# Optimization experiments

Measured on AMD Instinct MI355X. Metric: run time of the kernel, lower is better.

## Reference

```python
import jax, jax.numpy as jnp
import numpy as np
from jax import lax

N_HEADS = 8

def _rope(x, d, base=10000.0):
    # x: [b, h, t, c]; rotary on first d dims (neox rotate-half within d), rest passes through
    t = x.shape[2]
    theta = 1.0 / (base ** (jnp.arange(0, d, 2, dtype=jnp.float32) / d))  # [d//2]
    ang = jnp.arange(t, dtype=jnp.float32)[:, None] * theta[None, :]      # [t, d//2]
    ang = jnp.concatenate([ang, ang], axis=-1)                            # [t, d]
    cos, sin = jnp.cos(ang), jnp.sin(ang)
    xr, xp = x[..., :d], x[..., d:]
    neg = jnp.concatenate([-xr[..., d // 2:], xr[..., :d // 2]], axis=-1)
    return jnp.concatenate([xr * cos + neg * sin, xp], axis=-1)

def _conv1x1(x, W, b):
    # x [b,c,t], W [o,c,1]
    return jnp.einsum('oc,bct->bot', W[..., 0], x) + b[None, :, None]

def _conv1d(x, W, b):
    pad = W.shape[-1] // 2
    y = lax.conv_general_dilated(x, W, (1,), [(pad, pad)], dimension_numbers=('NCH', 'OIH', 'NCH'))
    return y + b[None, :, None]

def _layer_norm_c(x, gamma, beta, eps=1e-4):
    # channel-dim LayerNorm on [b,c,t]
    mean = jnp.mean(x, axis=1, keepdims=True)
    var = jnp.mean((x - mean) ** 2, axis=1, keepdims=True)
    return (x - mean) * lax.rsqrt(var + eps) * gamma[None, :, None] + beta[None, :, None]

def _forward(x, x_mask, Wq, bq, Wk, bk, Wv, bv, Wo, bo, g1, be1, W1, c1, W2, c2, g2, be2):
    B, C, T = x.shape
    H = N_HEADS
    kc = C // H
    d_rope = kc // 2
    scale = np.float32(1.0 / np.sqrt(kc))
    attn_mask = (x_mask[:, :, None, :] * x_mask[:, :, :, None]) > 0  # [B,1,T,T]

    def split(u):
        return u.reshape(B, H, kc, T).transpose(0, 1, 3, 2)  # b (h c) t -> b h t c

    for i in range(Wq.shape[0]):
        x = x * x_mask
        q = _rope(split(_conv1x1(x, Wq[i], bq[i])), d_rope)
        k = _rope(split(_conv1x1(x, Wk[i], bk[i])), d_rope)
        v = split(_conv1x1(x, Wv[i], bv[i]))
        scores = jnp.einsum('bhtc,bhsc->bhts', q, k) * scale
        scores = jnp.where(attn_mask, scores, jnp.float32(-10000.0))
        p = jax.nn.softmax(scores, axis=-1)
        o = jnp.einsum('bhts,bhsc->bhtc', p, v)
        o = o.transpose(0, 1, 3, 2).reshape(B, C, T)  # b h t c -> b (h c) t
        x = _layer_norm_c(x + _conv1x1(o, Wo[i], bo[i]), g1[i], be1[i])
        h = jax.nn.relu(_conv1d(x * x_mask, W1[i], c1[i]))
        y = _conv1d(h * x_mask, W2[i], c2[i]) * x_mask
        x = _layer_norm_c(x + y, g2[i], be2[i])
    return x * x_mask

def setup_inputs():
    key = jax.random.key(0)
    B, C, T, F, K, L = 4, 512, 1024, 2048, 3, 6
    ks = jax.random.split(key, 8)
    s = np.float32(1.0 / np.sqrt(C))
    return {
        'x': jax.random.normal(ks[0], (B, C, T), dtype=jnp.float32),
        'x_mask': jnp.ones((B, 1, T), dtype=jnp.float32),
        'Wq': jax.random.normal(ks[1], (L, C, C, 1), jnp.float32) * s,
        'bq': jnp.zeros((L, C), jnp.float32),
        'Wk': jax.random.normal(ks[2], (L, C, C, 1), jnp.float32) * s,
        'bk': jnp.zeros((L, C), jnp.float32),
        'Wv': jax.random.normal(ks[3], (L, C, C, 1), jnp.float32) * s,
        'bv': jnp.zeros((L, C), jnp.float32),
        'Wo': jax.random.normal(ks[4], (L, C, C, 1), jnp.float32) * s,
        'bo': jnp.zeros((L, C), jnp.float32),
        'g1': jnp.ones((L, C), jnp.float32),
        'be1': jnp.zeros((L, C), jnp.float32),
        'W1': jax.random.normal(ks[5], (L, F, C, K), jnp.float32) * np.float32(1.0 / np.sqrt(C * K)),
        'c1': jnp.zeros((L, F), jnp.float32),
        'W2': jax.random.normal(ks[6], (L, C, F, K), jnp.float32) * np.float32(1.0 / np.sqrt(F * K)),
        'c2': jnp.zeros((L, C), jnp.float32),
        'g2': jnp.ones((L, C), jnp.float32),
        'be2': jnp.zeros((L, C), jnp.float32),
    }

def reference(x, x_mask, Wq, bq, Wk, bk, Wv, bv, Wo, bo, g1, be1, W1, c1, W2, c2, g2, be2):
    return _forward(x, x_mask, Wq, bq, Wk, bk, Wv, bv, Wo, bo, g1, be1, W1, c1, W2, c2, g2, be2)
```

## Files before the change

### kernel.cpp

```cpp
#include <hip/hip_runtime.h>

typedef __bf16 bf16;
typedef __bf16 bf16x2 __attribute__((ext_vector_type(2)));
typedef __bf16 bf16x8 __attribute__((ext_vector_type(8)));
typedef __bf16 bf16x4v __attribute__((ext_vector_type(4)));
typedef float f32x4 __attribute__((ext_vector_type(4)));

constexpr int B = 4, C = 512, T = 1024, H = 8, F = 2048, L = 6;
constexpr int TP = T + 18;
constexpr float SCALE = 0.125f, EPS = 1e-4f;

__device__ __forceinline__ void stage_rows(const char* g, long strideB, char* lds,
                                           int nChunks, int tid) {
  const int wave = tid >> 6, lane = tid & 63;
  for (int c = wave; c < nChunks; c += 4) {
    int row = (c << 4) + (lane >> 2);
    int kq = (lane & 3) ^ ((row >> 1) & 3);
    const char* src = g + (long)row * strideB + kq * 16;
    char* dst = lds + ((long)c << 10);
    __builtin_amdgcn_global_load_lds((const __attribute__((address_space(1))) void*)src,
                                     (__attribute__((address_space(3))) void*)dst,
                                     16, 0, 0);
  }
}

__device__ __forceinline__ void stage_rows128(const char* g, long strideB, char* lds,
                                              int nChunks, int tid) {
  const int wave = tid >> 6, lane = tid & 63;
  for (int c = wave; c < nChunks; c += 4) {
    int row = (c << 3) + (lane >> 3);
    int kq = (lane & 7) ^ ((lane >> 3) & 7);
    const char* src = g + (long)row * strideB + kq * 16;
    char* dst = lds + ((long)c << 10);
    __builtin_amdgcn_global_load_lds((const __attribute__((address_space(1))) void*)src,
                                     (__attribute__((address_space(3))) void*)dst,
                                     16, 0, 0);
  }
}

template <int BM, int BN, int KW, int EPI, bool RELU, bool MASKM, int ZD,
          bool AZL, bool OZL, int MINW>
__global__ __launch_bounds__(256, MINW) void gemm_kernel(
    const bf16* __restrict__ A, const bf16* __restrict__ Bw,
    const float* __restrict__ bias, const float* __restrict__ mask,
    bf16* __restrict__ O, bf16* __restrict__ O2, bf16* __restrict__ O3,
    int lda, int ldb, int ldo, int K, long bSlice,
    long aZ1, long aZ2, long bZ1, long bZ2, long oZ1, long oZ2, int zoff,
    const float* __restrict__ ropeC, const float* __restrict__ ropeS)
{
  constexpr int WTM = BM / 2, WTN = BN / 2, FM = WTM / 16, FN = WTN / 16;
  constexpr int RA = (KW == 3) ? BM + 16 : BM;
  constexpr int ACH = RA / 16;
  constexpr int BCHS = BN / 16;
  constexpr int TCH = ACH + KW * BCHS;
  __shared__ __align__(1024) bf16 sBuf[2][TCH * 512];

  const int tid = threadIdx.x;
  const int zl = blockIdx.z, zg = zl + zoff;
  const int zb = zg / ZD, zh = zg % ZD;
  const long aOff = AZL ? (long)zl * aZ1 : (long)zb * aZ1 + (long)zh * aZ2;
  const long bOff = (long)zb * bZ1 + (long)zh * bZ2;
  const long oOff = OZL ? (long)zl * oZ1 : (long)zb * oZ1 + (long)zh * oZ2;
  const int m0 = blockIdx.x * BM, n0 = blockIdx.y * BN;
  const bf16* Ab = A + aOff + (long)m0 * lda;
  const bf16* Bb = Bw + bOff + (long)n0 * ldb;

  const int wid = tid >> 6, lane = tid & 63;
  const int wm = wid >> 1, wn = wid & 1;
  const int l16 = lane & 15, q4 = lane >> 4;

  f32x4 acc[FM][FN] = {};

  auto STAGE = [&](int k0, int buf) {
    char* sa = (char*)sBuf[buf];
    stage_rows((const char*)(Ab + k0), (long)lda * 2, sa, ACH, tid);
    #pragma unroll
    for (int kw = 0; kw < KW; ++kw)
      stage_rows((const char*)(Bb + (long)kw * bSlice + k0), (long)ldb * 2,
                 sa + (ACH + kw * BCHS) * 1024, BCHS, tid);
  };

  auto COMPUTE = [&](int buf) {
    const char* sa = (const char*)sBuf[buf];
    const char* sb = sa + ACH * 1024;
    #pragma unroll
    for (int kw = 0; kw < KW; ++kw) {
      bf16x8 af[FM], bfr[FN];
      #pragma unroll
      for (int fm = 0; fm < FM; ++fm) {
        int row = wm * WTM + fm * 16 + l16 + (KW == 3 ? kw : 0);
        unsigned ad = (unsigned)(row * 64 + q4 * 16);
        ad ^= ((ad >> 7) & 3u) << 4;
        af[fm] = *(const bf16x8*)(sa + ad);
      }
      #pragma unroll
      for (int fn = 0; fn < FN; ++fn) {
        int rn = wn * WTN + fn * 16 + l16;
        unsigned bd = (unsigned)(rn * 64 + q4 * 16);
        bd ^= ((bd >> 7) & 3u) << 4;
        bfr[fn] = *(const bf16x8*)(sb + kw * BCHS * 1024 + bd);
      }
      #pragma unroll
      for (int fm = 0; fm < FM; ++fm)
        #pragma unroll
        for (int fn = 0; fn < FN; ++fn)
          acc[fm][fn] = __builtin_amdgcn_mfma_f32_16x16x32_bf16(af[fm], bfr[fn],
                                                                acc[fm][fn], 0, 0, 0);
    }
  };

  STAGE(0, 0);
  __syncthreads();
  int cur = 0;
  for (int k0 = 32; k0 < K; k0 += 32) {
    STAGE(k0, cur ^ 1);
    COMPUTE(cur);
    __syncthreads();
    cur ^= 1;
  }
  COMPUTE(cur);

  float varr[FN][FM][4];
  #pragma unroll
  for (int fn = 0; fn < FN; ++fn) {
    const int nl = n0 + wn * WTN + fn * 16 + l16;
    const float bv = (bias == nullptr) ? 0.f : bias[nl];
    #pragma unroll
    for (int fm = 0; fm < FM; ++fm) {
      const int mb = m0 + wm * WTM + fm * 16 + q4 * 4;
      #pragma unroll
      for (int i = 0; i < 4; ++i) {
        float t = acc[fm][fn][i] + bv;
        if (RELU) t = fmaxf(t, 0.f);
        if (MASKM) t *= mask[(long)zb * T + mb + i];
        varr[fn][fm][i] = t;
      }
    }
  }

  if constexpr (EPI == 2) {
    if (n0 + wn * WTN < 1024) {
      #pragma unroll
      for (int fm = 0; fm < FM; ++fm) {
        const int mb = m0 + wm * WTM + fm * 16 + q4 * 4;
        #pragma unroll
        for (int i = 0; i < 4; ++i) {
          const int t = mb + i;
          float cv = ropeC[t * 16 + l16], sv = ropeS[t * 16 + l16];
          float a = varr[0][fm][i], b2 = varr[1][fm][i];
          varr[0][fm][i] = a * cv - b2 * sv;
          varr[1][fm][i] = b2 * cv + a * sv;
        }
      }
    }
  }

  #pragma unroll
  for (int fn = 0; fn < FN; ++fn) {
    const int nl = n0 + wn * WTN + fn * 16 + l16;
    #pragma unroll
    for (int fm = 0; fm < FM; ++fm) {
      const int mb = m0 + wm * WTM + fm * 16 + q4 * 4;
      if constexpr (EPI == 2) {
        if (nl < 1024) {
          bf16* dst = (nl < 512 ? O : O2) + oOff + (nl & 511);
          #pragma unroll
          for (int i = 0; i < 4; ++i)
            dst[(long)(mb + i) * C] = (bf16)varr[fn][fm][i];
        } else {
          bf16x4v tv;
          #pragma unroll
          for (int i = 0; i < 4; ++i) tv[i] = (bf16)varr[fn][fm][i];
          *(bf16x4v*)(O3 + oOff + (long)(nl - 1024) * T + mb) = tv;
        }
      } else {
        bf16* dst = O + oOff;
        #pragma unroll
        for (int i = 0; i < 4; ++i)
          dst[(long)(mb + i) * ldo + nl] = (bf16)varr[fn][fm][i];
      }
    }
  }
}

__global__ __launch_bounds__(256, 3) void flash_kernel(
    const bf16* __restrict__ q, const bf16* __restrict__ k,
    const bf16* __restrict__ vT, const float* __restrict__ mask,
    bf16* __restrict__ o)
{
  __shared__ __align__(1024) char sQ[64 * 128];
  __shared__ __align__(1024) char sK[2][64 * 128];
  __shared__ __align__(1024) char sV[2][64 * 128];
  __shared__ __align__(1024) char sP[4][16 * 128];

  const int tid = threadIdx.x;
  const int w = tid >> 6, lane = tid & 63;
  const int l16 = lane & 15, q4 = lane >> 4;
  const int q0 = blockIdx.x * 64;
  const int bh = blockIdx.y;
  const int b = bh >> 3, h = bh & 7;

  const bf16* qb = q + ((long)b * T + q0) * C + h * 64;
  const bf16* kb = k + (long)b * T * C + h * 64;
  const bf16* vb = vT + (long)b * C * T + (long)h * 64 * T;

  stage_rows128((const char*)qb, (long)C * 2, sQ, 8, tid);
  stage_rows128((const char*)kb, (long)C * 2, sK[0], 8, tid);
  stage_rows128((const char*)vb, (long)T * 2, sV[0], 8, tid);
  __syncthreads();

  bf16x8 af_q[2];
  {
    const int r = w * 16 + l16;
    #pragma unroll
    for (int kk = 0; kk < 2; ++kk) {
      unsigned off = (unsigned)(kk * 64 + q4 * 16) ^ ((unsigned)(r & 7) << 4);
      af_q[kk] = *(const bf16x8*)(sQ + r * 128 + off);
    }
  }

  float mq[4];
  #pragma unroll
  for (int i = 0; i < 4; ++i)
    mq[i] = mask[(long)b * T + q0 + w * 16 + q4 * 4 + i];

  f32x4 accO[4] = {};
  float mrun[4] = {-1e30f, -1e30f, -1e30f, -1e30f};
  float lrun[4] = {0.f, 0.f, 0.f, 0.f};
  char* sPw = sP[w];

  int cur = 0;
  for (int it = 0; it < 16; ++it) {
    if (it < 15) {
      stage_rows128((const char*)(kb + (long)(it + 1) * 64 * C), (long)C * 2, sK[cur ^ 1], 8, tid);
      stage_rows128((const char*)(vb + (it + 1) * 64), (long)T * 2, sV[cur ^ 1], 8, tid);
    }
    f32x4 s[4] = {};
    #pragma unroll
    for (int kk = 0; kk < 2; ++kk) {
      #pragma unroll
      for (int fn = 0; fn < 4; ++fn) {
        const int rn = fn * 16 + l16;
        unsigned off = (unsigned)(kk * 64 + q4 * 16) ^ ((unsigned)(rn & 7) << 4);
        bf16x8 kf = *(const bf16x8*)(sK[cur] + rn * 128 + off);
        s[fn] = __builtin_amdgcn_mfma_f32_16x16x32_bf16(af_q[kk], kf, s[fn], 0, 0, 0);
      }
    }
    float mk[4];
    #pragma unroll
    for (int fn = 0; fn < 4; ++fn)
      mk[fn] = mask[(long)b * T + it * 64 + fn * 16 + l16];
    float sv[4][4];
    #pragma unroll
    for (int fn = 0; fn < 4; ++fn)
      #pragma unroll
      for (int i = 0; i < 4; ++i) {
        float xval = s[fn][i] * SCALE;
        sv[fn][i] = (mq[i] * mk[fn] > 0.f) ? xval : -10000.f;
      }
    float cor[4];
    #pragma unroll
    for (int i = 0; i < 4; ++i) {
      float m0 = fmaxf(fmaxf(sv[0][i], sv[1][i]), fmaxf(sv[2][i], sv[3][i]));
      #pragma unroll
      for (int st = 1; st < 16; st <<= 1) m0 = fmaxf(m0, __shfl_xor(m0, st, 64));
      float mnew = fmaxf(mrun[i], m0);
      cor[i] = __expf(mrun[i] - mnew);
      mrun[i] = mnew;
    }
    float rs[4] = {0.f, 0.f, 0.f, 0.f};
    #pragma unroll
    for (int fn = 0; fn < 4; ++fn)
      #pragma unroll
      for (int i = 0; i < 4; ++i) {
        float p = __expf(sv[fn][i] - mrun[i]);
        rs[i] += p;
        const int row = q4 * 4 + i;
        unsigned off = (unsigned)((fn * 16 + l16) * 2) ^ ((unsigned)(row & 7) << 4);
        *(bf16*)(sPw + row * 128 + off) = (bf16)p;
      }
    #pragma unroll
    for (int i = 0; i < 4; ++i) {
      #pragma unroll
      for (int st = 1; st < 16; st <<= 1) rs[i] += __shfl_xor(rs[i], st, 64);
      lrun[i] = lrun[i] * cor[i] + rs[i];
    }
    #pragma unroll
    for (int fn = 0; fn < 4; ++fn)
      #pragma unroll
      for (int i = 0; i < 4; ++i) accO[fn][i] *= cor[i];
    #pragma unroll
    for (int kk = 0; kk < 2; ++kk) {
      unsigned poff = (unsigned)(kk * 64 + q4 * 16) ^ ((unsigned)(l16 & 7) << 4);
      bf16x8 pf = *(const bf16x8*)(sPw + l16 * 128 + poff);
      #pragma unroll
      for (int fn = 0; fn < 4; ++fn) {
        const int rn = fn * 16 + l16;
        unsigned off = (unsigned)(kk * 64 + q4 * 16) ^ ((unsigned)(rn & 7) << 4);
        bf16x8 vf = *(const bf16x8*)(sV[cur] + rn * 128 + off);
        accO[fn] = __builtin_amdgcn_mfma_f32_16x16x32_bf16(pf, vf, accO[fn], 0, 0, 0);
      }
    }
    __syncthreads();
    cur ^= 1;
  }

  float linv[4];
  #pragma unroll
  for (int i = 0; i < 4; ++i) linv[i] = 1.f / lrun[i];
  #pragma unroll
  for (int fn = 0; fn < 4; ++fn)
    #pragma unroll
    for (int i = 0; i < 4; ++i)
      o[((long)b * T + q0 + w * 16 + q4 * 4 + i) * C + h * 64 + fn * 16 + l16] =
          (bf16)(accO[fn][i] * linv[i]);
}

__global__ __launch_bounds__(256) void rope_tab_kernel(float* __restrict__ cosT,
                                                       float* __restrict__ sinT) {
  int idx = blockIdx.x * 256 + threadIdx.x;
  if (idx >= T * 16) return;
  int t = idx >> 4, j = idx & 15;
  float theta = powf(10000.f, -(float)j / 16.f);
  float s, c;
  sincosf((float)t * theta, &s, &c);
  cosT[idx] = c;
  sinT[idx] = s;
}

__global__ __launch_bounds__(256) void ln_kernel(
    const float* __restrict__ x, const bf16* __restrict__ y,
    const float* __restrict__ gamma, const float* __restrict__ beta,
    const float* __restrict__ mask, int maskA, int maskY,
    float* __restrict__ xout, bf16* __restrict__ xm)
{
  const int w = threadIdx.x >> 6, lane = threadIdx.x & 63;
  const long row = (long)blockIdx.x * 4 + w;
  const int b = (int)(row >> 10), t = (int)(row & 1023);
  const float* xr = x + row * C;
  const bf16* yr = y + row * C;
  const float m = mask[(long)b * T + t];
  const float fa = maskA ? m : 1.f, fy = maskY ? m : 1.f;
  float4 x0 = *(const float4*)(xr + lane * 8);
  float4 x1 = *(const float4*)(xr + lane * 8 + 4);
  bf16x8 yv = *(const bf16x8*)(yr + lane * 8);
  float vals[8] = {x0.x, x0.y, x0.z, x0.w, x1.x, x1.y, x1.z, x1.w};
  float sum = 0.f, sq = 0.f;
  #pragma unroll
  for (int i = 0; i < 8; ++i) {
    vals[i] = vals[i] * fa + (float)yv[i] * fy;
    sum += vals[i]; sq += vals[i] * vals[i];
  }
  #pragma unroll
  for (int s = 1; s < 64; s <<= 1) {
    sum += __shfl_xor(sum, s, 64);
    sq  += __shfl_xor(sq, s, 64);
  }
  float mean = sum * (1.f / C);
  float rstd = rsqrtf(sq * (1.f / C) - mean * mean + EPS);
  float4 g0 = *(const float4*)(gamma + lane * 8), g1v = *(const float4*)(gamma + lane * 8 + 4);
  float4 b0 = *(const float4*)(beta + lane * 8),  b1v = *(const float4*)(beta + lane * 8 + 4);
  float gg[8] = {g0.x, g0.y, g0.z, g0.w, g1v.x, g1v.y, g1v.z, g1v.w};
  float bb[8] = {b0.x, b0.y, b0.z, b0.w, b1v.x, b1v.y, b1v.z, b1v.w};
  float o[8]; bf16x8 xmv;
  #pragma unroll
  for (int i = 0; i < 8; ++i) {
    o[i] = (vals[i] - mean) * rstd * gg[i] + bb[i];
    xmv[i] = (bf16)(o[i] * m);
  }
  *(float4*)(xout + row * C + lane * 8)     = make_float4(o[0], o[1], o[2], o[3]);
  *(float4*)(xout + row * C + lane * 8 + 4) = make_float4(o[4], o[5], o[6], o[7]);
  *(bf16x8*)(xm + ((long)b * TP + t + 1) * C + lane * 8) = xmv;
}

__global__ __launch_bounds__(256) void transpose_in_kernel(const float* __restrict__ xin,
                                                           const float* __restrict__ mask,
                                                           float* __restrict__ x,
                                                           bf16* __restrict__ xm) {
  __shared__ float tile[32][33];
  int tx = threadIdx.x, ty = threadIdx.y;
  int t0 = blockIdx.x * 32, c0 = blockIdx.y * 32, b = blockIdx.z;
  #pragma unroll
  for (int i = 0; i < 4; ++i)
    tile[ty + i * 8][tx] = xin[((long)b * C + c0 + ty + i * 8) * T + t0 + tx];
  __syncthreads();
  #pragma unroll
  for (int i = 0; i < 4; ++i) {
    int t = t0 + ty + i * 8;
    float val = tile[tx][ty + i * 8];
    float m = mask[(long)b * T + t];
    x[((long)b * T + t) * C + c0 + tx] = val;
    xm[((long)b * TP + t + 1) * C + c0 + tx] = (bf16)(val * m);
  }
}

__global__ __launch_bounds__(256) void transpose_out_kernel(const float* __restrict__ x,
                                                            const float* __restrict__ mask,
                                                            float* __restrict__ out) {
  __shared__ float tile[32][33];
  int tx = threadIdx.x, ty = threadIdx.y;
  int t0 = blockIdx.x * 32, c0 = blockIdx.y * 32, b = blockIdx.z;
  #pragma unroll
  for (int i = 0; i < 4; ++i)
    tile[ty + i * 8][tx] = x[((long)b * T + t0 + ty + i * 8) * C + c0 + tx];
  __syncthreads();
  #pragma unroll
  for (int i = 0; i < 4; ++i) {
    int t = t0 + tx;
    out[((long)b * C + c0 + ty + i * 8) * T + t] = tile[tx][ty + i * 8] * mask[(long)b * T + t];
  }
}

__global__ __launch_bounds__(256) void zero_pads_kernel(bf16* __restrict__ xm, bf16* __restrict__ h) {
  long idx = (long)blockIdx.x * 256 + threadIdx.x;
  const long n1 = (long)B * 18 * C;
  const long n2 = (long)B * 18 * F;
  if (idx < n1) {
    int c = (int)(idx % C); int r = (int)((idx / C) % 18); int b = (int)(idx / (18L * C));
    int p = (r == 0) ? 0 : (T + r);
    xm[((long)b * TP + p) * C + c] = (bf16)0.f;
  } else if (idx < n1 + n2) {
    long j = idx - n1;
    int c = (int)(j % F); int r = (int)((j / F) % 18); int b = (int)(j / (18L * F));
    int p = (r == 0) ? 0 : (T + r);
    h[((long)b * TP + p) * F + c] = (bf16)0.f;
  }
}

__global__ __launch_bounds__(256) void cvt_qkv_all(const float* __restrict__ Wq,
                                                   const float* __restrict__ Wk,
                                                   const float* __restrict__ Wv,
                                                   bf16* __restrict__ dst) {
  long idx = (long)blockIdx.x * 256 + threadIdx.x;
  if (idx >= (long)L * 3 * C * C / 4) return;
  int c4 = (int)(idx & 127) * 4;
  int n = (int)((idx >> 7) & 511);
  int s2 = (int)(idx >> 16);
  int slot = s2 % 3, i = s2 / 3;
  const float* src = (slot == 0 ? Wq : slot == 1 ? Wk : Wv) + (long)i * C * C + (long)n * C + c4;
  float4 v = *(const float4*)src;
  bf16x4v d = {(bf16)v.x, (bf16)v.y, (bf16)v.z, (bf16)v.w};
  *(bf16x4v*)(dst + (((long)(i * 3 + slot) * 512 + n) * 512 + c4)) = d;
}

__global__ __launch_bounds__(256) void cvt_wo_all(const float* __restrict__ src,
                                                  bf16* __restrict__ dst) {
  long idx = (long)blockIdx.x * 256 + threadIdx.x;
  if (idx >= (long)L * C * C / 4) return;
  float4 v = *(const float4*)(src + idx * 4);
  bf16x4v d = {(bf16)v.x, (bf16)v.y, (bf16)v.z, (bf16)v.w};
  *(bf16x4v*)(dst + idx * 4) = d;
}

__global__ __launch_bounds__(256) void cvt_w3_all(const float* __restrict__ src,
                                                  bf16* __restrict__ dst, int N, int Kd) {
  long idx = (long)blockIdx.x * 256 + threadIdx.x;
  long total = (long)L * N * Kd / 2;
  if (idx >= total) return;
  const int half = Kd >> 1;
  int c2 = (int)(idx % half) * 2;
  long r = idx / half;
  int n = (int)(r % N);
  int i = (int)(r / N);
  const float* s = src + ((long)i * N * Kd + (long)n * Kd + c2) * 3;
  float v0 = s[0], v1 = s[1], v2 = s[2], v3 = s[3], v4 = s[4], v5 = s[5];
  long plane = (long)N * Kd;
  long baseo = (long)i * 3 * plane + (long)n * Kd + c2;
  bf16x2 d0 = {(bf16)v0, (bf16)v3};
  bf16x2 d1 = {(bf16)v1, (bf16)v4};
  bf16x2 d2 = {(bf16)v2, (bf16)v5};
  *(bf16x2*)(dst + baseo)             = d0;
  *(bf16x2*)(dst + baseo + plane)     = d1;
  *(bf16x2*)(dst + baseo + 2 * plane) = d2;
}

__global__ __launch_bounds__(256) void cvt_bias_all(const float* __restrict__ bq,
                                                    const float* __restrict__ bk,
                                                    const float* __restrict__ bv,
                                                    float* __restrict__ dst) {
  int idx = blockIdx.x * 256 + threadIdx.x;
  if (idx >= L * 1536) return;
  int j = idx % 1536, i = idx / 1536;
  float v = (j < 512) ? bq[i * 512 + j] : (j < 1024) ? bk[i * 512 + j - 512]
                                                     : bv[i * 512 + j - 1024];
  dst[idx] = v;
}

extern "C" void kernel_launch(void* const* d_in, const int* in_sizes, int n_in,
                              void* d_out, int out_size, void* d_ws, size_t ws_size,
                              hipStream_t stream)
{
  const float* xin = (const float*)d_in[0];
  const float* msk = (const float*)d_in[1];
  const float* Wq  = (const float*)d_in[2];
  const float* bq  = (const float*)d_in[3];
  const float* Wk  = (const float*)d_in[4];
  const float* bk  = (const float*)d_in[5];
  const float* Wv  = (const float*)d_in[6];
  const float* bv  = (const float*)d_in[7];
  const float* Wo  = (const float*)d_in[8];
  const float* bo  = (const float*)d_in[9];
  const float* g1  = (const float*)d_in[10];
  const float* be1 = (const float*)d_in[11];
  const float* W1  = (const float*)d_in[12];
  const float* c1  = (const float*)d_in[13];
  const float* W2  = (const float*)d_in[14];
  const float* c2  = (const float*)d_in[15];
  const float* g2  = (const float*)d_in[16];
  const float* be2 = (const float*)d_in[17];

  size_t off = 0;
  char* base = (char*)d_ws;
  auto alloc = [&](size_t bytes) -> char* {
    char* r = base + off;
    off = (off + bytes + 1023) & ~(size_t)1023;
    return r;
  };
  float* x     = (float*)alloc((size_t)B * T * C * 4);
  float* ropeC = (float*)alloc((size_t)T * 16 * 4);
  float* ropeS = (float*)alloc((size_t)T * 16 * 4);
  bf16* xm  = (bf16*)alloc((size_t)B * TP * C * 2);
  bf16* hb  = (bf16*)alloc((size_t)B * TP * F * 2);
  bf16* q   = (bf16*)alloc((size_t)B * T * C * 2);
  bf16* k   = (bf16*)alloc((size_t)B * T * C * 2);
  bf16* vT  = (bf16*)alloc((size_t)B * T * C * 2);
  bf16* o   = (bf16*)alloc((size_t)B * T * C * 2);
  bf16* yb  = (bf16*)alloc((size_t)B * T * C * 2);
  bf16* wqkv_all = (bf16*)alloc((size_t)L * 3 * C * C * 2);
  bf16* wo_all   = (bf16*)alloc((size_t)L * C * C * 2);
  bf16* w1_all   = (bf16*)alloc((size_t)L * 3 * F * C * 2);
  bf16* w2_all   = (bf16*)alloc((size_t)L * 3 * C * F * 2);
  float* bqkv_all = (float*)alloc((size_t)L * 1536 * 4);
  (void)in_sizes; (void)n_in; (void)out_size; (void)ws_size;

  {
    long tot = (long)B * 18 * (C + F);
    zero_pads_kernel<<<(int)((tot + 255) / 256), 256, 0, stream>>>(xm, hb);
  }
  transpose_in_kernel<<<dim3(T / 32, C / 32, B), dim3(32, 8), 0, stream>>>(xin, msk, x, xm);
  rope_tab_kernel<<<(T * 16 + 255) / 256, 256, 0, stream>>>(ropeC, ropeS);
  cvt_qkv_all<<<(int)(((long)L * 3 * C * C / 4 + 255) / 256), 256, 0, stream>>>(Wq, Wk, Wv, wqkv_all);
  cvt_wo_all<<<(int)(((long)L * C * C / 4 + 255) / 256), 256, 0, stream>>>(Wo, wo_all);
  cvt_w3_all<<<(int)(((long)L * F * C / 2 + 255) / 256), 256, 0, stream>>>(W1, w1_all, F, C);
  cvt_w3_all<<<(int)(((long)L * C * F / 2 + 255) / 256), 256, 0, stream>>>(W2, w2_all, C, F);
  cvt_bias_all<<<(L * 1536 + 255) / 256, 256, 0, stream>>>(bq, bk, bv, bqkv_all);

  for (int i = 0; i < L; ++i) {
    const bf16* wqkv = wqkv_all + (long)i * 3 * C * C;
    const bf16* wo   = wo_all + (long)i * C * C;
    const bf16* w1b  = w1_all + (long)i * 3 * F * C;
    const bf16* w2b  = w2_all + (long)i * 3 * C * F;
    const float* bqkv = bqkv_all + (long)i * 1536;

    gemm_kernel<64, 128, 1, 2, false, false, 1, false, false, 4>
        <<<dim3(16, 12, B), 256, 0, stream>>>(
        xm + C, wqkv, bqkv, msk, q, k, vT,
        C, C, C, C, 0,
        (long)TP * C, 0, 0, 0, (long)T * C, 0, 0, ropeC, ropeS);

    flash_kernel<<<dim3(T / 64, B * H), 256, 0, stream>>>(q, k, vT, msk, o);

    gemm_kernel<64, 64, 1, 0, false, false, 1, false, false, 4>
        <<<dim3(64, 8, 1), 256, 0, stream>>>(
        o, wo, bo + (size_t)i * C, msk, yb, nullptr, nullptr,
        C, C, C, C, 0,
        0, 0, 0, 0, 0, 0, 0, nullptr, nullptr);

    ln_kernel<<<B * T / 4, 256, 0, stream>>>(x, yb, g1 + (size_t)i * C, be1 + (size_t)i * C,
                                             msk, 1, 0, x, xm);

    gemm_kernel<128, 128, 3, 0, true, true, 1, false, false, 2>
        <<<dim3(8, 16, B), 256, 0, stream>>>(
        xm, w1b, c1 + (size_t)i * F, msk, hb + F, nullptr, nullptr,
        C, C, F, C, (long)F * C,
        (long)TP * C, 0, 0, 0, (long)TP * F, 0, 0, nullptr, nullptr);

    gemm_kernel<64, 64, 3, 0, false, false, 1, false, false, 4>
        <<<dim3(16, 8, B), 256, 0, stream>>>(
        hb, w2b, c2 + (size_t)i * C, msk, yb, nullptr, nullptr,
        F, F, C, F, (long)C * F,
        (long)TP * F, 0, 0, 0, (long)T * C, 0, 0, nullptr, nullptr);

    ln_kernel<<<B * T / 4, 256, 0, stream>>>(x, yb, g2 + (size_t)i * C, be2 + (size_t)i * C,
                                             msk, 0, 1, x, xm);
  }

  transpose_out_kernel<<<dim3(T / 32, C / 32, B), dim3(32, 8), 0, stream>>>(x, msk, (float*)d_out);
}
```

Measured before the change: 904.8 us.

## Add triple-buffered LDS pipeline with vmcnt waits to small GEMMs

Adds a three-stage LDS ring buffer to the GEMM kernel, keeping two tiles of global-to-LDS loads in flight and waiting on a counted vmcnt instead of a full __syncthreads drain. Chunk counts are padded to a multiple of the wave count so every wave issues the same number of loads, which keeps the vmcnt literal correct. This is enabled for the QKV, output-projection and second FFN GEMMs; the first FFN GEMM stays double-buffered. The goal is to hide global load latency behind MFMA work, at the cost of more LDS per block (possibly lower occupancy) and some redundant padded loads.

```diff
diff --git a/kernel.cpp b/kernel.cpp
--- a/kernel.cpp
+++ b/kernel.cpp
@@ -10,14 +10,28 @@
 constexpr int TP = T + 18;
 constexpr float SCALE = 0.125f, EPS = 1e-4f;
 
-__device__ __forceinline__ void stage_rows(const char* g, long strideB, char* lds,
-                                           int nChunks, int tid) {
+template <int N> __device__ __forceinline__ void vmcnt_wait() {
+  if constexpr (N == 0)       asm volatile("s_waitcnt vmcnt(0)" ::: "memory");
+  else if constexpr (N == 2)  asm volatile("s_waitcnt vmcnt(2)" ::: "memory");
+  else if constexpr (N == 3)  asm volatile("s_waitcnt vmcnt(3)" ::: "memory");
+  else if constexpr (N == 4)  asm volatile("s_waitcnt vmcnt(4)" ::: "memory");
+  else if constexpr (N == 5)  asm volatile("s_waitcnt vmcnt(5)" ::: "memory");
+  else if constexpr (N == 6)  asm volatile("s_waitcnt vmcnt(6)" ::: "memory");
+  else if constexpr (N == 8)  asm volatile("s_waitcnt vmcnt(8)" ::: "memory");
+  else if constexpr (N == 10) asm volatile("s_waitcnt vmcnt(10)" ::: "memory");
+  else if constexpr (N == 12) asm volatile("s_waitcnt vmcnt(12)" ::: "memory");
+  else static_assert(N == 0, "unsupported vmcnt literal");
+}
+
+__device__ __forceinline__ void stage_rows_p(const char* g, long strideB, char* lds,
+                                             int nC, int nCP, int tid) {
   const int wave = tid >> 6, lane = tid & 63;
-  for (int c = wave; c < nChunks; c += 4) {
-    int row = (c << 4) + (lane >> 2);
+  for (int c = wave; c < nCP; c += 4) {
+    int cc = (c < nC) ? c : (c - nC);
+    int row = (cc << 4) + (lane >> 2);
     int kq = (lane & 3) ^ ((row >> 1) & 3);
     const char* src = g + (long)row * strideB + kq * 16;
-    char* dst = lds + ((long)c << 10);
+    char* dst = lds + ((long)cc << 10);
     __builtin_amdgcn_global_load_lds((const __attribute__((address_space(1))) void*)src,
                                      (__attribute__((address_space(3))) void*)dst,
                                      16, 0, 0);
@@ -39,7 +53,7 @@
 }
 
 template <int BM, int BN, int KW, int EPI, bool RELU, bool MASKM, int ZD,
-          bool AZL, bool OZL, int MINW>
+          bool AZL, bool OZL, int MINW, int NBUF>
 __global__ __launch_bounds__(256, MINW) void gemm_kernel(
     const bf16* __restrict__ A, const bf16* __restrict__ Bw,
     const float* __restrict__ bias, const float* __restrict__ mask,
@@ -53,7 +67,10 @@
   constexpr int ACH = RA / 16;
   constexpr int BCHS = BN / 16;
   constexpr int TCH = ACH + KW * BCHS;
-  __shared__ __align__(1024) bf16 sBuf[2][TCH * 512];
+  constexpr int ACHP = (ACH + 3) & ~3;
+  constexpr int BCHSP = (BCHS + 3) & ~3;
+  constexpr int CHW = ACHP / 4 + KW * (BCHSP / 4);
+  __shared__ __align__(1024) bf16 sBuf[NBUF][TCH * 512];
 
   const int tid = threadIdx.x;
   const int zl = blockIdx.z, zg = zl + zoff;
@@ -73,11 +90,13 @@
 
   auto STAGE = [&](int k0, int buf) {
     char* sa = (char*)sBuf[buf];
-    stage_rows((const char*)(Ab + k0), (long)lda * 2, sa, ACH, tid);
+    stage_rows_p((const char*)(Ab + k0), (long)lda * 2, sa, ACH,
+                 NBUF == 3 ? ACHP : ACH, tid);
     #pragma unroll
     for (int kw = 0; kw < KW; ++kw)
-      stage_rows((const char*)(Bb + (long)kw * bSlice + k0), (long)ldb * 2,
-                 sa + (ACH + kw * BCHS) * 1024, BCHS, tid);
+      stage_rows_p((const char*)(Bb + (long)kw * bSlice + k0), (long)ldb * 2,
+                   sa + (ACH + kw * BCHS) * 1024, BCHS,
+                   NBUF == 3 ? BCHSP : BCHS, tid);
   };
 
   auto COMPUTE = [&](int buf) {
@@ -109,16 +128,36 @@
     }
   };
 
-  STAGE(0, 0);
-  __syncthreads();
-  int cur = 0;
-  for (int k0 = 32; k0 < K; k0 += 32) {
-    STAGE(k0, cur ^ 1);
+  if constexpr (NBUF == 3) {
+    STAGE(0, 0);
+    STAGE(32, 1);
+    int cur = 0;
+    for (int k0 = 0; k0 < K; k0 += 32) {
+      if (k0 + 64 < K) STAGE(k0 + 64, cur == 0 ? 2 : cur - 1);
+      const int rem = K - k0;
+      if (rem > 64)      vmcnt_wait<2 * CHW>();
+      else if (rem > 32) vmcnt_wait<CHW>();
+      else               vmcnt_wait<0>();
+      __builtin_amdgcn_s_barrier();
+      __builtin_amdgcn_sched_barrier(0);
+      COMPUTE(cur);
+      __builtin_amdgcn_sched_barrier(0);
+      __builtin_amdgcn_s_barrier();
+      __builtin_amdgcn_sched_barrier(0);
+      cur = (cur == 2) ? 0 : cur + 1;
+    }
+  } else {
+    STAGE(0, 0);
+    __syncthreads();
+    int cur = 0;
+    for (int k0 = 32; k0 < K; k0 += 32) {
+      STAGE(k0, cur ^ 1);
+      COMPUTE(cur);
+      __syncthreads();
+      cur ^= 1;
+    }
     COMPUTE(cur);
-    __syncthreads();
-    cur ^= 1;
-  }
-  COMPUTE(cur);
+  }
 
   float varr[FN][FM][4];
   #pragma unroll
@@ -552,7 +591,7 @@
     const bf16* w2b  = w2_all + (long)i * 3 * C * F;
     const float* bqkv = bqkv_all + (long)i * 1536;
 
-    gemm_kernel<64, 128, 1, 2, false, false, 1, false, false, 4>
+    gemm_kernel<64, 128, 1, 2, false, false, 1, false, false, 4, 3>
         <<<dim3(16, 12, B), 256, 0, stream>>>(
         xm + C, wqkv, bqkv, msk, q, k, vT,
         C, C, C, C, 0,
@@ -560,7 +599,7 @@
 
     flash_kernel<<<dim3(T / 64, B * H), 256, 0, stream>>>(q, k, vT, msk, o);
 
-    gemm_kernel<64, 64, 1, 0, false, false, 1, false, false, 4>
+    gemm_kernel<64, 64, 1, 0, false, false, 1, false, false, 4, 3>
         <<<dim3(64, 8, 1), 256, 0, stream>>>(
         o, wo, bo + (size_t)i * C, msk, yb, nullptr, nullptr,
         C, C, C, C, 0,
@@ -569,13 +608,13 @@
     ln_kernel<<<B * T / 4, 256, 0, stream>>>(x, yb, g1 + (size_t)i * C, be1 + (size_t)i * C,
                                              msk, 1, 0, x, xm);
 
-    gemm_kernel<128, 128, 3, 0, true, true, 1, false, false, 2>
+    gemm_kernel<128, 128, 3, 0, true, true, 1, false, false, 2, 2>
         <<<dim3(8, 16, B), 256, 0, stream>>>(
         xm, w1b, c1 + (size_t)i * F, msk, hb + F, nullptr, nullptr,
         C, C, F, C, (long)F * C,
         (long)TP * C, 0, 0, 0, (long)TP * F, 0, 0, nullptr, nullptr);
 
-    gemm_kernel<64, 64, 3, 0, false, false, 1, false, false, 4>
+    gemm_kernel<64, 64, 3, 0, false, false, 1, false, false, 4, 3>
         <<<dim3(16, 8, B), 256, 0, stream>>>(
         hb, w2b, c2 + (size_t)i * C, msk, yb, nullptr, nullptr,
         F, F, C, F, (long)C * F,
```

After: 949.7 us. 5.0% more time.

## Split-K the FFN down-projection GEMM into two fp32 halves summed in LayerNorm

Applied to the files above, without the earlier changes.

The second FFN conv GEMM (K = 3*F) now runs as a split-K of 2 over the grid z dimension, with each half writing fp32 partials to a new workspace buffer and only the first half adding the bias. The following LayerNorm kernel gains a template mode that reads and sums both fp32 partials instead of a bf16 result. This doubles the block count of a small 128-block-per-batch GEMM to improve occupancy on the device, at the cost of extra fp32 write and read traffic for the partials.

```diff
diff --git a/kernel.cpp b/kernel.cpp
--- a/kernel.cpp
+++ b/kernel.cpp
@@ -124,7 +124,7 @@
   #pragma unroll
   for (int fn = 0; fn < FN; ++fn) {
     const int nl = n0 + wn * WTN + fn * 16 + l16;
-    const float bv = (bias == nullptr) ? 0.f : bias[nl];
+    const float bv = (bias == nullptr || (EPI == 3 && zh != 0)) ? 0.f : bias[nl];
     #pragma unroll
     for (int fm = 0; fm < FM; ++fm) {
       const int mb = m0 + wm * WTM + fm * 16 + q4 * 4;
@@ -173,6 +173,11 @@
           for (int i = 0; i < 4; ++i) tv[i] = (bf16)varr[fn][fm][i];
           *(bf16x4v*)(O3 + oOff + (long)(nl - 1024) * T + mb) = tv;
         }
+      } else if constexpr (EPI == 3) {
+        float* dst = (float*)O + oOff;
+        #pragma unroll
+        for (int i = 0; i < 4; ++i)
+          dst[(long)(mb + i) * ldo + nl] = varr[fn][fm][i];
       } else {
         bf16* dst = O + oOff;
         #pragma unroll
@@ -328,8 +333,10 @@
   sinT[idx] = s;
 }
 
+template <bool SPLITY>
 __global__ __launch_bounds__(256) void ln_kernel(
     const float* __restrict__ x, const bf16* __restrict__ y,
+    const float* __restrict__ yf,
     const float* __restrict__ gamma, const float* __restrict__ beta,
     const float* __restrict__ mask, int maskA, int maskY,
     float* __restrict__ xout, bf16* __restrict__ xm)
@@ -338,17 +345,28 @@
   const long row = (long)blockIdx.x * 4 + w;
   const int b = (int)(row >> 10), t = (int)(row & 1023);
   const float* xr = x + row * C;
-  const bf16* yr = y + row * C;
   const float m = mask[(long)b * T + t];
   const float fa = maskA ? m : 1.f, fy = maskY ? m : 1.f;
   float4 x0 = *(const float4*)(xr + lane * 8);
   float4 x1 = *(const float4*)(xr + lane * 8 + 4);
-  bf16x8 yv = *(const bf16x8*)(yr + lane * 8);
   float vals[8] = {x0.x, x0.y, x0.z, x0.w, x1.x, x1.y, x1.z, x1.w};
+  float yv[8];
+  if constexpr (SPLITY) {
+    const float* y0 = yf + row * C + lane * 8;
+    const float* y1 = y0 + (long)B * T * C;
+    float4 a0 = *(const float4*)y0, a1 = *(const float4*)(y0 + 4);
+    float4 b0 = *(const float4*)y1, b1 = *(const float4*)(y1 + 4);
+    yv[0] = a0.x + b0.x; yv[1] = a0.y + b0.y; yv[2] = a0.z + b0.z; yv[3] = a0.w + b0.w;
+    yv[4] = a1.x + b1.x; yv[5] = a1.y + b1.y; yv[6] = a1.z + b1.z; yv[7] = a1.w + b1.w;
+  } else {
+    bf16x8 yb = *(const bf16x8*)(y + row * C + lane * 8);
+    #pragma unroll
+    for (int i = 0; i < 8; ++i) yv[i] = (float)yb[i];
+  }
   float sum = 0.f, sq = 0.f;
   #pragma unroll
   for (int i = 0; i < 8; ++i) {
-    vals[i] = vals[i] * fa + (float)yv[i] * fy;
+    vals[i] = vals[i] * fa + yv[i] * fy;
     sum += vals[i]; sq += vals[i] * vals[i];
   }
   #pragma unroll
@@ -526,6 +544,7 @@
   bf16* vT  = (bf16*)alloc((size_t)B * T * C * 2);
   bf16* o   = (bf16*)alloc((size_t)B * T * C * 2);
   bf16* yb  = (bf16*)alloc((size_t)B * T * C * 2);
+  float* yb32 = (float*)alloc((size_t)2 * B * T * C * 4);
   bf16* wqkv_all = (bf16*)alloc((size_t)L * 3 * C * C * 2);
   bf16* wo_all   = (bf16*)alloc((size_t)L * C * C * 2);
   bf16* w1_all   = (bf16*)alloc((size_t)L * 3 * F * C * 2);
@@ -566,8 +585,8 @@
         C, C, C, C, 0,
         0, 0, 0, 0, 0, 0, 0, nullptr, nullptr);
 
-    ln_kernel<<<B * T / 4, 256, 0, stream>>>(x, yb, g1 + (size_t)i * C, be1 + (size_t)i * C,
-                                             msk, 1, 0, x, xm);
+    ln_kernel<false><<<B * T / 4, 256, 0, stream>>>(
+        x, yb, nullptr, g1 + (size_t)i * C, be1 + (size_t)i * C, msk, 1, 0, x, xm);
 
     gemm_kernel<128, 128, 3, 0, true, true, 1, false, false, 2>
         <<<dim3(8, 16, B), 256, 0, stream>>>(
@@ -575,14 +594,15 @@
         C, C, F, C, (long)F * C,
         (long)TP * C, 0, 0, 0, (long)TP * F, 0, 0, nullptr, nullptr);
 
-    gemm_kernel<64, 64, 3, 0, false, false, 1, false, false, 4>
-        <<<dim3(16, 8, B), 256, 0, stream>>>(
-        hb, w2b, c2 + (size_t)i * C, msk, yb, nullptr, nullptr,
-        F, F, C, F, (long)C * F,
-        (long)TP * F, 0, 0, 0, (long)T * C, 0, 0, nullptr, nullptr);
-
-    ln_kernel<<<B * T / 4, 256, 0, stream>>>(x, yb, g2 + (size_t)i * C, be2 + (size_t)i * C,
-                                             msk, 0, 1, x, xm);
+    gemm_kernel<64, 64, 3, 3, false, false, 2, false, false, 4>
+        <<<dim3(16, 8, 2 * B), 256, 0, stream>>>(
+        hb, w2b, c2 + (size_t)i * C, msk, (bf16*)yb32, nullptr, nullptr,
+        F, F, C, F / 2, (long)C * F,
+        (long)TP * F, (long)(F / 2), 0, (long)(F / 2),
+        (long)T * C, (long)B * T * C, 0, nullptr, nullptr);
+
+    ln_kernel<true><<<B * T / 4, 256, 0, stream>>>(
+        x, nullptr, yb32, g2 + (size_t)i * C, be2 + (size_t)i * C, msk, 0, 1, x, xm);
   }
 
   transpose_out_kernel<<<dim3(T / 32, C / 32, B), dim3(32, 8), 0, stream>>>(x, msk, (float*)d_out);
```

New measurement: 950.0 us. +5.0%, slower.
